# Kernel tuning notes

Measured on AMD Instinct MI355X. Metric: run time of the kernel, lower is better.

The kernel has to match this reference:

```python
import jax, jax.numpy as jnp
import numpy as np

GRID_INTERVAL = 0.3  # grid_interval init arg (used as module-level global in the original source)
EPS = 1e-12
B, G, M, N_ORB, DIM = 16, 4096, 128, 400, 768


def setup_inputs() -> dict:
    key = jax.random.key(0)
    k1, k2, k3, k4, k5 = jax.random.split(key, 5)
    # distances are physical (positive); avoid d=0 so negative powers in the laplace GTO stay finite
    distance_matrices = jax.random.uniform(k1, (B, G, M), jnp.float32, 0.5, 8.0)
    quantum_numbers = jax.random.randint(k2, (B, M), 0, 3).astype(jnp.int32) + 1  # principal q in {1,2,3}
    atomic_orbitals = jax.random.randint(k3, (B, M), 0, N_ORB)
    N_electrons = jax.random.uniform(k4, (B,), jnp.float32, 2.0, 68.0)
    coefficient_table = jax.random.normal(k5, (N_ORB, DIM), jnp.float32)  # nn.Embedding(N_orbitals, dim)
    zeta_table = jnp.ones((N_ORB, 1), jnp.float32)  # nn.Embedding(N_orbitals, 1), init ones
    return dict(distance_matrices=distance_matrices,
                quantum_numbers=quantum_numbers,
                atomic_orbitals=atomic_orbitals,
                N_electrons=N_electrons,
                coefficient_table=coefficient_table,
                zeta_table=zeta_table)


def _gto_bases(d, q, z):
    """GTO and laplace-GTO basis matrices, normalized over the grid axis.
    d: [B,G,M] distances; q: [B,1,M] principal quantum numbers (float); z: [B,1,M] zetas.
    Block-diagonal pad value 1e6 in the original makes off-block entries exactly 0,
    so the per-molecule batched norm over axis=1 matches the block-diagonal column norm.
    """
    e = jnp.exp(-(z ** 2) * d ** 2)
    gto = d ** (q - 1.0) * e  # d^(q-1) * exp(-z^2 d^2)
    denom = jnp.maximum(jnp.linalg.norm(gto, axis=1, keepdims=True), EPS) * GRID_INTERVAL ** 1.5
    l_gto = d ** (q - 3.0) * e * (4.0 * z ** 4 * d ** 4
                                  - 2.0 * z ** 2 * (2.0 * q + 1.0) * d ** 2
                                  + q * (q - 1.0))
    return gto / denom, l_gto / denom


def reference(distance_matrices, quantum_numbers, atomic_orbitals, N_electrons,
              coefficient_table, zeta_table):
    Bv, Gv, Mv = distance_matrices.shape
    D = coefficient_table.shape[1]
    q = quantum_numbers.astype(distance_matrices.dtype)[:, None, :]      # [B,1,M]
    z = zeta_table[atomic_orbitals][..., 0][:, None, :]                  # [B,1,M]
    n_gto, n_l_gto = _gto_bases(distance_matrices, q, z)                 # [B,G,M]
    # LCAO coefficients: F.normalize(coefficient(AOs), 2, 0) per molecule (norm over orbital axis M)
    c = coefficient_table[atomic_orbitals]                               # [B,M,D]
    c = c / jnp.maximum(jnp.linalg.norm(c, axis=1, keepdims=True), EPS)
    mo = jnp.einsum('bgm,bmd->bgd', n_gto, c)                            # molecular orbitals
    l_mo = jnp.einsum('bgm,bmd->bgd', n_l_gto, c)                        # laplace MOs
    # normalize MOs per molecule over the grid axis, scale by sqrt(N_el/dim); laplace MOs share denom
    denom = jnp.maximum(jnp.linalg.norm(mo, axis=1, keepdims=True), EPS)
    scale = jnp.sqrt(N_electrons / D)[:, None, None]
    mo_n = scale * mo / denom
    l_mo_n = scale * l_mo / denom
    # torch.cat over molecules along the grid axis -> [B*G, D]; stack (MOs, laplace MOs)
    return jnp.stack([mo_n.reshape(Bv * Gv, D), l_mo_n.reshape(Bv * Gv, D)])
```

## Files before the change

kernel.cpp:

```cpp
#include <hip/hip_runtime.h>
#include <hip/hip_bf16.h>
#include <math.h>

#define B_    16
#define G_    4096
#define M_    128
#define D_    768
#define GI15  0.16431676725154983f
#define EPS_  1e-12f

typedef __attribute__((ext_vector_type(8))) short short8v;
typedef __attribute__((ext_vector_type(4))) float f32x4;
typedef unsigned short ushort_t;
typedef unsigned int   uint_t;

__device__ __forceinline__ ushort_t f2bf(float f) {
    uint_t u = __float_as_uint(f);
    u += 0x7FFFu + ((u >> 16) & 1u);
    return (ushort_t)(u >> 16);
}
__device__ __forceinline__ float bf2f(ushort_t h) {
    return __uint_as_float(((uint_t)h) << 16);
}

__global__ __launch_bounds__(256) void k_gram_part(
        const float* __restrict__ dist,
        const int*   __restrict__ qn,
        const int*   __restrict__ ao,
        const float* __restrict__ zeta,
        float*       __restrict__ part) {
    __shared__ float sg[64][M_];
    __shared__ float pz2[M_], pq[M_];
    const int b = blockIdx.y, ch = blockIdx.x, tid = threadIdx.x;
    if (tid < M_) {
        pq[tid] = (float)qn[b * M_ + tid];
        float z = zeta[ao[b * M_ + tid]];
        pz2[tid] = z * z;
    }
    __syncthreads();
    {
        int m = tid & 127;
        float z2 = pz2[m], q = pq[m];
        for (int r = tid >> 7; r < 64; r += 2) {
            float d = dist[((size_t)(b * G_ + ch * 64 + r)) * M_ + m];
            float e  = __expf(-z2 * d * d);
            float p1 = (q < 1.5f) ? 1.f : ((q < 2.5f) ? d : d * d);
            sg[r][m] = p1 * e;
        }
    }
    __syncthreads();
    const int mi0 = (tid >> 4) * 8;
    const int mj0 = (tid & 15) * 8;
    float acc[8][8];
    #pragma unroll
    for (int i = 0; i < 8; ++i)
        #pragma unroll
        for (int j = 0; j < 8; ++j) acc[i][j] = 0.f;
    #pragma unroll 2
    for (int g = 0; g < 64; ++g) {
        float av[8], bv[8];
        *(float4*)&av[0] = *(const float4*)&sg[g][mi0];
        *(float4*)&av[4] = *(const float4*)&sg[g][mi0 + 4];
        *(float4*)&bv[0] = *(const float4*)&sg[g][mj0];
        *(float4*)&bv[4] = *(const float4*)&sg[g][mj0 + 4];
        #pragma unroll
        for (int i = 0; i < 8; ++i)
            #pragma unroll
            for (int j = 0; j < 8; ++j)
                acc[i][j] = fmaf(av[i], bv[j], acc[i][j]);
    }
    float* pp = part + ((size_t)(ch * B_ + b)) * (M_ * M_);
    #pragma unroll
    for (int i = 0; i < 8; ++i) {
        *(float4*)&pp[(mi0 + i) * M_ + mj0]     = make_float4(acc[i][0], acc[i][1], acc[i][2], acc[i][3]);
        *(float4*)&pp[(mi0 + i) * M_ + mj0 + 4] = make_float4(acc[i][4], acc[i][5], acc[i][6], acc[i][7]);
    }
}

__global__ void k_gram_red(const float* __restrict__ part,
                           float*       __restrict__ gram) {
    int idx = blockIdx.x * 256 + threadIdx.x;
    float s = 0.f;
    #pragma unroll 8
    for (int ch = 0; ch < 64; ++ch)
        s += part[(size_t)ch * (B_ * M_ * M_) + idx];
    gram[idx] = s;
}

__global__ __launch_bounds__(256) void k_mosq(
        const float* __restrict__ gram,
        const int*   __restrict__ ao,
        const float* __restrict__ table,
        const float* __restrict__ Nel,
        ushort_t*    __restrict__ bhiG,
        ushort_t*    __restrict__ bloG) {
    __shared__ float sv[M_][64];
    __shared__ float sGq[32][M_];
    __shared__ float prg[M_];
    __shared__ float sred[4][64];
    __shared__ float srcn[64], scf[64];
    const int b = blockIdx.y, d0 = blockIdx.x * 64, tid = threadIdx.x;
    const int dl = tid & 63, quad = tid >> 6;
    const float* gb = gram + (size_t)b * M_ * M_;
    if (tid < M_)
        prg[tid] = 1.f / (fmaxf(sqrtf(gb[tid * M_ + tid]), EPS_) * GI15);
    #pragma unroll 4
    for (int k = 0; k < 32; ++k) {
        int m = quad * 32 + k;
        sv[m][dl] = table[(size_t)ao[b * M_ + m] * D_ + d0 + dl];
    }
    __syncthreads();
    {
        float cs = 0.f;
        #pragma unroll 4
        for (int k = 0; k < 32; ++k) { float v = sv[quad * 32 + k][dl]; cs = fmaf(v, v, cs); }
        sred[quad][dl] = cs;
    }
    __syncthreads();
    if (quad == 0)
        srcn[dl] = 1.f / fmaxf(sqrtf(sred[0][dl] + sred[1][dl] + sred[2][dl] + sred[3][dl]), EPS_);
    #pragma unroll 4
    for (int k = 0; k < 32; ++k) { int m = quad * 32 + k; sv[m][dl] *= prg[m]; }
    __syncthreads();
    float acc = 0.f;
    for (int qt = 0; qt < 4; ++qt) {
        for (int e = tid; e < 32 * M_; e += 256)
            sGq[e >> 7][e & 127] = gb[(qt * 32 + (e >> 7)) * M_ + (e & 127)];
        __syncthreads();
        #pragma unroll
        for (int mr8 = 0; mr8 < 8; ++mr8) {
            int mr = quad * 8 + mr8;
            float t0 = 0.f, t1 = 0.f, t2 = 0.f, t3 = 0.f;
            #pragma unroll 4
            for (int mc = 0; mc < M_; mc += 4) {
                t0 = fmaf(sGq[mr][mc],     sv[mc][dl],     t0);
                t1 = fmaf(sGq[mr][mc + 1], sv[mc + 1][dl], t1);
                t2 = fmaf(sGq[mr][mc + 2], sv[mc + 2][dl], t2);
                t3 = fmaf(sGq[mr][mc + 3], sv[mc + 3][dl], t3);
            }
            acc = fmaf(sv[qt * 32 + mr][dl], (t0 + t1) + (t2 + t3), acc);
        }
        __syncthreads();
    }
    sred[quad][dl] = acc;
    __syncthreads();
    if (quad == 0) {
        float qf  = fmaxf(sred[0][dl] + sred[1][dl] + sred[2][dl] + sred[3][dl], 0.f);
        float rcn = srcn[dl];
        float mo  = rcn * sqrtf(qf);
        scf[dl] = sqrtf(Nel[b] / (float)D_) / fmaxf(mo, EPS_) * rcn;
    }
    __syncthreads();
    {
        float cfv = scf[dl];
        ushort_t* bh = bhiG + ((size_t)b * D_ + d0 + dl) * M_;
        ushort_t* bl = bloG + ((size_t)b * D_ + d0 + dl) * M_;
        #pragma unroll
        for (int mq = 0; mq < 4; ++mq) {
            int mb = quad * 32 + mq * 8;
            ushort_t h[8], l[8];
            #pragma unroll
            for (int r = 0; r < 8; ++r) {
                float v = sv[mb + r][dl] * cfv;
                h[r] = f2bf(v);
                l[r] = f2bf(v - bf2f(h[r]));
            }
            *(uint4*)&bh[mb] = *(const uint4*)&h[0];
            *(uint4*)&bl[mb] = *(const uint4*)&l[0];
        }
    }
}

__global__ __launch_bounds__(512, 4) void k_gemm(
        const float* __restrict__ dist,
        const int*   __restrict__ qn,
        const int*   __restrict__ ao,
        const float* __restrict__ zeta,
        const ushort_t* __restrict__ bhiG,
        const ushort_t* __restrict__ bloG,
        float*       __restrict__ out) {
    __shared__ ushort_t sA0[2048], sA1[2048], sA2[2048], sA3[2048];
    __shared__ ushort_t sBh[16384], sBl[16384];
    const int tid = threadIdx.x;
    const int b  = blockIdx.z;
    const int g0 = blockIdx.y * 64;
    const int d0 = blockIdx.x * 128;

    {
        const uint_t* gh = (const uint_t*)(bhiG + ((size_t)b * D_ + d0) * M_);
        const uint_t* gl = (const uint_t*)(bloG + ((size_t)b * D_ + d0) * M_);
        #pragma unroll
        for (int p = 0; p < 16; ++p) {
            int j = p * 512 + tid;
            int drow   = j >> 6;
            int inrow4 = (j & 63) << 2;
            int tgt = drow * 256 + (inrow4 ^ ((drow & 7) << 4));
            *(uint_t*)((char*)sBh + tgt) = gh[j];
            *(uint_t*)((char*)sBl + tgt) = gl[j];
        }
    }

    const int ml  = tid & 31;
    const int gof = tid >> 5;
    float q4[4], z24[4];
    #pragma unroll
    for (int kc = 0; kc < 4; ++kc) {
        int m = kc * 32 + ml;
        q4[kc]  = (float)qn[b * M_ + m];
        float z = zeta[ao[b * M_ + m]];
        z24[kc] = z * z;
    }

    const int lane = tid & 63, w = tid >> 6;
    const int gsub  = (w & 3) * 16;
    const int dhalf = (w >> 2) * 64;
    const int lrow = lane & 15, lk8 = (lane >> 4) * 8;
    f32x4 accm[4], accl[4];
    #pragma unroll
    for (int t = 0; t < 4; ++t) {
        accm[t] = (f32x4){0.f, 0.f, 0.f, 0.f};
        accl[t] = (f32x4){0.f, 0.f, 0.f, 0.f};
    }
    __syncthreads();

    for (int kc = 0; kc < 4; ++kc) {
        {
            int m = kc * 32 + ml;
            float z2 = z24[kc], q = q4[kc];
            float c4 = 4.f * z2 * z2;
            float c2 = 2.f * z2 * (2.f * q + 1.f);
            float c0 = q * (q - 1.f);
            #pragma unroll
            for (int pass = 0; pass < 4; ++pass) {
                int g = pass * 16 + gof;
                float d  = dist[((size_t)(b * G_ + g0 + g)) * M_ + m];
                float d2 = d * d;
                float e  = __expf(-z2 * d2);
                float p1 = (q < 1.5f) ? 1.f : ((q < 2.5f) ? d : d2);
                float gto  = p1 * e;
                float poly = fmaf(fmaf(c4, d2, -c2), d2, c0);
                float lg   = __fdividef(p1, d2) * e * poly;
                int o = g * 32 + ml;
                ushort_t gh = f2bf(gto);
                sA0[o] = gh;
                sA1[o] = f2bf(gto - bf2f(gh));
                ushort_t lh = f2bf(lg);
                sA2[o] = lh;
                sA3[o] = f2bf(lg - bf2f(lh));
            }
        }
        __syncthreads();
        {
            int oa = (gsub + lrow) * 32 + lk8;
            short8v agh = *(const short8v*)&sA0[oa];
            short8v agl = *(const short8v*)&sA1[oa];
            short8v alh = *(const short8v*)&sA2[oa];
            short8v all_= *(const short8v*)&sA3[oa];
            int kk2 = (kc * 32 + lk8) * 2;
            #pragma unroll
            for (int dt = 0; dt < 4; ++dt) {
                int dr = dhalf + dt * 16 + lrow;
                int off = dr * 256 + (kk2 ^ ((dr & 7) << 4));
                short8v bh = *(const short8v*)((const char*)sBh + off);
                short8v bl = *(const short8v*)((const char*)sBl + off);
                accm[dt] = __builtin_amdgcn_mfma_f32_16x16x32_bf16(agh, bh, accm[dt], 0, 0, 0);
                accm[dt] = __builtin_amdgcn_mfma_f32_16x16x32_bf16(agh, bl, accm[dt], 0, 0, 0);
                accm[dt] = __builtin_amdgcn_mfma_f32_16x16x32_bf16(agl, bh, accm[dt], 0, 0, 0);
                accl[dt] = __builtin_amdgcn_mfma_f32_16x16x32_bf16(alh, bh, accl[dt], 0, 0, 0);
                accl[dt] = __builtin_amdgcn_mfma_f32_16x16x32_bf16(alh, bl, accl[dt], 0, 0, 0);
                accl[dt] = __builtin_amdgcn_mfma_f32_16x16x32_bf16(all_, bh, accl[dt], 0, 0, 0);
            }
        }
        __syncthreads();
    }

    const size_t HALF = (size_t)B_ * G_ * D_;
    const int grow = g0 + gsub + (lane >> 4) * 4;
    #pragma unroll
    for (int dt = 0; dt < 4; ++dt) {
        int dcol = d0 + dhalf + dt * 16 + lrow;
        #pragma unroll
        for (int r = 0; r < 4; ++r) {
            size_t off = ((size_t)(b * G_) + grow + r) * D_ + dcol;
            out[off]        = accm[dt][r];
            out[HALF + off] = accl[dt][r];
        }
    }
}

extern "C" void kernel_launch(void* const* d_in, const int* in_sizes, int n_in,
                              void* d_out, int out_size, void* d_ws, size_t ws_size,
                              hipStream_t stream) {
    const float* dist  = (const float*)d_in[0];
    const int*   qn    = (const int*)  d_in[1];
    const int*   ao    = (const int*)  d_in[2];
    const float* Nel   = (const float*)d_in[3];
    const float* table = (const float*)d_in[4];
    const float* zeta  = (const float*)d_in[5];
    float* out = (float*)d_out;
    float* ws  = (float*)d_ws;

    float*    gram = ws;
    ushort_t* bhi  = (ushort_t*)(ws + 262144);
    ushort_t* blo  = (ushort_t*)(ws + 262144 + 786432);
    float*    part = out;

    k_gram_part<<<dim3(64, B_), 256, 0, stream>>>(dist, qn, ao, zeta, part);
    k_gram_red<<<1024, 256, 0, stream>>>(part, gram);
    k_mosq<<<dim3(D_ / 64, B_), 256, 0, stream>>>(gram, ao, table, Nel, bhi, blo);
    k_gemm<<<dim3(D_ / 128, G_ / 64, B_), 512, 0, stream>>>(
        dist, qn, ao, zeta, bhi, blo, out);
}
```

Baseline: 590.5 us.

## Precompute split-bf16 GTO basis in separate kernel and stream it into GEMM

Adds a kernel that computes the GTO and laplace-GTO values once per (g,m), splits each into hi/lo bf16, and writes them to workspace in MFMA-fragment order. The GEMM kernel then loads A fragments directly from global memory instead of recomputing exp and conversions in every d-tile block. This removes the per-kc LDS staging and its syncs. Before, that work was repeated across 6 d-blocks. The cost is an extra 32 MB write and read of A data plus one more kernel launch.

```diff
diff --git a/kernel.cpp b/kernel.cpp
--- a/kernel.cpp
+++ b/kernel.cpp
@@ -21,6 +21,43 @@
 }
 __device__ __forceinline__ float bf2f(ushort_t h) {
     return __uint_as_float(((uint_t)h) << 16);
+}
+
+__global__ __launch_bounds__(256) void k_agen(
+        const float* __restrict__ dist,
+        const int*   __restrict__ qn,
+        const int*   __restrict__ ao,
+        const float* __restrict__ zeta,
+        ushort_t*    __restrict__ A4) {
+    const int b = blockIdx.y, gb = blockIdx.x, tid = threadIdx.x;
+    const int m = tid & 127, gh2 = tid >> 7;
+    const float q  = (float)qn[b * M_ + m];
+    const float z  = zeta[ao[b * M_ + m]];
+    const float z2 = z * z;
+    const float c4 = 4.f * z2 * z2;
+    const float c2 = 2.f * z2 * (2.f * q + 1.f);
+    const float c0 = q * (q - 1.f);
+    const int kc = m >> 5, k = m & 31;
+    ushort_t* base = A4 + ((((size_t)(b * 64 + gb)) * 4 + kc) * 4) * 2048 + k;
+    const float* dp = dist + ((size_t)(b * G_ + gb * 64 + gh2)) * M_ + m;
+    #pragma unroll 4
+    for (int r = 0; r < 32; ++r) {
+        int g = r * 2 + gh2;
+        float d  = dp[(size_t)(r * 2) * M_];
+        float d2 = d * d;
+        float e  = __expf(-z2 * d2);
+        float p1 = (q < 1.5f) ? 1.f : ((q < 2.5f) ? d : d2);
+        float gto  = p1 * e;
+        float poly = fmaf(fmaf(c4, d2, -c2), d2, c0);
+        float lg   = __fdividef(p1, d2) * e * poly;
+        ushort_t gh = f2bf(gto);
+        ushort_t lh = f2bf(lg);
+        ushort_t* p = base + g * 32;
+        p[0]    = gh;
+        p[2048] = f2bf(gto - bf2f(gh));
+        p[4096] = lh;
+        p[6144] = f2bf(lg - bf2f(lh));
+    }
 }
 
 __global__ __launch_bounds__(256) void k_gram_part(
@@ -172,14 +209,10 @@
 }
 
 __global__ __launch_bounds__(512, 4) void k_gemm(
-        const float* __restrict__ dist,
-        const int*   __restrict__ qn,
-        const int*   __restrict__ ao,
-        const float* __restrict__ zeta,
+        const ushort_t* __restrict__ A4,
         const ushort_t* __restrict__ bhiG,
         const ushort_t* __restrict__ bloG,
         float*       __restrict__ out) {
-    __shared__ ushort_t sA0[2048], sA1[2048], sA2[2048], sA3[2048];
     __shared__ ushort_t sBh[16384], sBl[16384];
     const int tid = threadIdx.x;
     const int b  = blockIdx.z;
@@ -200,17 +233,6 @@
         }
     }
 
-    const int ml  = tid & 31;
-    const int gof = tid >> 5;
-    float q4[4], z24[4];
-    #pragma unroll
-    for (int kc = 0; kc < 4; ++kc) {
-        int m = kc * 32 + ml;
-        q4[kc]  = (float)qn[b * M_ + m];
-        float z = zeta[ao[b * M_ + m]];
-        z24[kc] = z * z;
-    }
-
     const int lane = tid & 63, w = tid >> 6;
     const int gsub  = (w & 3) * 16;
     const int dhalf = (w >> 2) * 64;
@@ -221,57 +243,31 @@
         accm[t] = (f32x4){0.f, 0.f, 0.f, 0.f};
         accl[t] = (f32x4){0.f, 0.f, 0.f, 0.f};
     }
-    __syncthreads();
-
+    const ushort_t* Ab = A4 + ((size_t)(b * 64 + blockIdx.y)) * 32768
+                            + (gsub + lrow) * 32 + lk8;
+    __syncthreads();
+
+    #pragma unroll
     for (int kc = 0; kc < 4; ++kc) {
-        {
-            int m = kc * 32 + ml;
-            float z2 = z24[kc], q = q4[kc];
-            float c4 = 4.f * z2 * z2;
-            float c2 = 2.f * z2 * (2.f * q + 1.f);
-            float c0 = q * (q - 1.f);
-            #pragma unroll
-            for (int pass = 0; pass < 4; ++pass) {
-                int g = pass * 16 + gof;
-                float d  = dist[((size_t)(b * G_ + g0 + g)) * M_ + m];
-                float d2 = d * d;
-                float e  = __expf(-z2 * d2);
-                float p1 = (q < 1.5f) ? 1.f : ((q < 2.5f) ? d : d2);
-                float gto  = p1 * e;
-                float poly = fmaf(fmaf(c4, d2, -c2), d2, c0);
-                float lg   = __fdividef(p1, d2) * e * poly;
-                int o = g * 32 + ml;
-                ushort_t gh = f2bf(gto);
-                sA0[o] = gh;
-                sA1[o] = f2bf(gto - bf2f(gh));
-                ushort_t lh = f2bf(lg);
-                sA2[o] = lh;
-                sA3[o] = f2bf(lg - bf2f(lh));
-            }
-        }
-        __syncthreads();
-        {
-            int oa = (gsub + lrow) * 32 + lk8;
-            short8v agh = *(const short8v*)&sA0[oa];
-            short8v agl = *(const short8v*)&sA1[oa];
-            short8v alh = *(const short8v*)&sA2[oa];
-            short8v all_= *(const short8v*)&sA3[oa];
-            int kk2 = (kc * 32 + lk8) * 2;
-            #pragma unroll
-            for (int dt = 0; dt < 4; ++dt) {
-                int dr = dhalf + dt * 16 + lrow;
-                int off = dr * 256 + (kk2 ^ ((dr & 7) << 4));
-                short8v bh = *(const short8v*)((const char*)sBh + off);
-                short8v bl = *(const short8v*)((const char*)sBl + off);
-                accm[dt] = __builtin_amdgcn_mfma_f32_16x16x32_bf16(agh, bh, accm[dt], 0, 0, 0);
-                accm[dt] = __builtin_amdgcn_mfma_f32_16x16x32_bf16(agh, bl, accm[dt], 0, 0, 0);
-                accm[dt] = __builtin_amdgcn_mfma_f32_16x16x32_bf16(agl, bh, accm[dt], 0, 0, 0);
-                accl[dt] = __builtin_amdgcn_mfma_f32_16x16x32_bf16(alh, bh, accl[dt], 0, 0, 0);
-                accl[dt] = __builtin_amdgcn_mfma_f32_16x16x32_bf16(alh, bl, accl[dt], 0, 0, 0);
-                accl[dt] = __builtin_amdgcn_mfma_f32_16x16x32_bf16(all_, bh, accl[dt], 0, 0, 0);
-            }
-        }
-        __syncthreads();
+        const ushort_t* Ak = Ab + kc * 8192;
+        short8v agh = *(const short8v*)&Ak[0];
+        short8v agl = *(const short8v*)&Ak[2048];
+        short8v alh = *(const short8v*)&Ak[4096];
+        short8v all_= *(const short8v*)&Ak[6144];
+        int kk2 = (kc * 32 + lk8) * 2;
+        #pragma unroll
+        for (int dt = 0; dt < 4; ++dt) {
+            int dr = dhalf + dt * 16 + lrow;
+            int off = dr * 256 + (kk2 ^ ((dr & 7) << 4));
+            short8v bh = *(const short8v*)((const char*)sBh + off);
+            short8v bl = *(const short8v*)((const char*)sBl + off);
+            accm[dt] = __builtin_amdgcn_mfma_f32_16x16x32_bf16(agh, bh, accm[dt], 0, 0, 0);
+            accm[dt] = __builtin_amdgcn_mfma_f32_16x16x32_bf16(agh, bl, accm[dt], 0, 0, 0);
+            accm[dt] = __builtin_amdgcn_mfma_f32_16x16x32_bf16(agl, bh, accm[dt], 0, 0, 0);
+            accl[dt] = __builtin_amdgcn_mfma_f32_16x16x32_bf16(alh, bh, accl[dt], 0, 0, 0);
+            accl[dt] = __builtin_amdgcn_mfma_f32_16x16x32_bf16(alh, bl, accl[dt], 0, 0, 0);
+            accl[dt] = __builtin_amdgcn_mfma_f32_16x16x32_bf16(all_, bh, accl[dt], 0, 0, 0);
+        }
     }
 
     const size_t HALF = (size_t)B_ * G_ * D_;
@@ -298,16 +294,17 @@
     const float* table = (const float*)d_in[4];
     const float* zeta  = (const float*)d_in[5];
     float* out = (float*)d_out;
-    float* ws  = (float*)d_ws;
-
-    float*    gram = ws;
-    ushort_t* bhi  = (ushort_t*)(ws + 262144);
-    ushort_t* blo  = (ushort_t*)(ws + 262144 + 786432);
+    char*  wsb = (char*)d_ws;
+
+    float*    gram = (float*)wsb;
+    ushort_t* bhi  = (ushort_t*)(wsb + (size_t)(1u << 20));
+    ushort_t* blo  = (ushort_t*)(wsb + (size_t)(4u << 20));
+    ushort_t* A4   = (ushort_t*)(wsb + (size_t)(8u << 20));
     float*    part = out;
 
+    k_agen<<<dim3(64, B_), 256, 0, stream>>>(dist, qn, ao, zeta, A4);
     k_gram_part<<<dim3(64, B_), 256, 0, stream>>>(dist, qn, ao, zeta, part);
     k_gram_red<<<1024, 256, 0, stream>>>(part, gram);
     k_mosq<<<dim3(D_ / 64, B_), 256, 0, stream>>>(gram, ao, table, Nel, bhi, blo);
-    k_gemm<<<dim3(D_ / 128, G_ / 64, B_), 512, 0, stream>>>(
-        dist, qn, ao, zeta, bhi, blo, out);
-}
+    k_gemm<<<dim3(D_ / 128, G_ / 64, B_), 512, 0, stream>>>(A4, bhi, blo, out);
+}
```

After: 621.5 us. +5.3%, slower.
